# Kernel optimization log

Hardware: AMD Instinct MI355X
Metric: run time of the kernel (lower is better)

Reference implementation:

```python
import jax, jax.numpy as jnp
import numpy as np

V = 10000   # vocab size
H = 768     # HIDDEN_SIZE
B = 8       # batch
S = 512     # padded seq len
L = 8       # TRANSFORMER_LAYERS
EPS = 1e-5  # torch LayerNorm default eps


def setup_inputs() -> dict:
    key = jax.random.key(0)
    ks = jax.random.split(key, 16)
    init = lambda k, shape: jax.random.normal(k, shape, jnp.float32) * 0.02
    x = jax.random.randint(ks[0], (B, S), 0, V)
    # full-length sequences: avoids NaN from the original's softmax(dim=1) over
    # fully -inf padded columns (same behavior as torch for this input)
    lengths = jnp.full((B,), S, dtype=jnp.int32)
    return {
        'x': x,
        'lengths': lengths,
        'emb_w': init(ks[1], (V, H)),
        'Wq': init(ks[2], (L, H, H)), 'bq': jnp.zeros((L, H), jnp.float32),
        'Wk': init(ks[3], (L, H, H)), 'bk': jnp.zeros((L, H), jnp.float32),
        'Wv': init(ks[4], (L, H, H)), 'bv': jnp.zeros((L, H), jnp.float32),
        'W1': init(ks[5], (L, H, H)), 'b1': jnp.zeros((L, H), jnp.float32),
        'W2': init(ks[6], (L, H, H)), 'b2': jnp.zeros((L, H), jnp.float32),
        'g1': jnp.ones((L, H), jnp.float32), 'be1': jnp.zeros((L, H), jnp.float32),
        'g2': jnp.ones((L, H), jnp.float32), 'be2': jnp.zeros((L, H), jnp.float32),
        'fc_w': init(ks[7], (H, H)), 'fc_b': jnp.zeros((H,), jnp.float32),
    }


def _layernorm(x, g, b):
    m = jnp.mean(x, axis=-1, keepdims=True)
    v = jnp.mean(jnp.square(x - m), axis=-1, keepdims=True)
    return (x - m) * jax.lax.rsqrt(v + EPS) * g + b


def _pos_encoding(seq, dim):
    pos = jnp.arange(seq, dtype=jnp.float32)[:, None]
    div = jnp.exp(jnp.arange(0, dim, 2, dtype=jnp.float32) * (-np.log(10000.0) / dim))
    ang = pos * div[None, :]                                  # [S, H/2]
    return jnp.stack([jnp.sin(ang), jnp.cos(ang)], axis=-1).reshape(seq, dim)


def reference(x, lengths, emb_w, Wq, bq, Wk, bk, Wv, bv, W1, b1, W2, b2,
              g1, be1, g2, be2, fc_w, fc_b):
    z = emb_w[x] + _pos_encoding(S, H)[None]                  # [B,S,H]
    causal = jnp.tril(jnp.ones((S, S), bool))                 # [S,S]
    valid = jnp.arange(S)[None, :] < lengths[:, None]         # [B,S]
    mask = causal[None] & valid[:, None, :] & valid[:, :, None]  # [B,S,S]
    scale = 1.0 / jnp.sqrt(jnp.float32(H))
    for i in range(L):
        q = z @ Wq[i] + bq[i]
        k = z @ Wk[i] + bk[i]
        v = z @ Wv[i] + bv[i]
        scores = jnp.einsum('bqh,bkh->bqk', q, k) * scale
        scores = jnp.where(mask, scores, -jnp.inf)
        # NOTE: original code applies softmax over dim=1 (query axis) — faithful
        atten = jax.nn.softmax(scores, axis=1)
        out = jnp.einsum('bqk,bkh->bqh', atten, v)
        o1 = _layernorm(z + out, g1[i], be1[i])               # eval: dropout=identity
        mid = jax.nn.relu(o1 @ W1[i] + b1[i]) @ W2[i] + b2[i]
        z = _layernorm(mid + o1, g2[i], be2[i])
    zf = z @ fc_w + fc_b                                      # [B,S,H]
    logits = jnp.einsum('bsh,vh->bsv', zf, emb_w)             # [B,S,V]
    return jax.nn.softmax(logits, axis=-1)
```

## Files before the change

### kernel.cpp

```cpp
#include <hip/hip_runtime.h>
#include <math.h>

typedef unsigned int   u32;
typedef unsigned short u16;
typedef __attribute__((ext_vector_type(8))) short bf16x8;
typedef __attribute__((ext_vector_type(4))) float f32x4;
typedef __attribute__((ext_vector_type(4))) unsigned short u16x4;
typedef __attribute__((ext_vector_type(8))) unsigned short u16x8;

#define HID   768
#define SEQ   512
#define BATCH 8
#define LAYERS 8
#define VOC   10000
#define NROWS (BATCH*SEQ)
#define NH    ((long long)NROWS*HID)
#define SS8   ((long long)BATCH*SEQ*SEQ)
#define EPSLN 1e-5f
#define WSZ   ((long long)HID*HID)

__device__ __forceinline__ u16 f2bf(float f) {
    u32 u = __builtin_bit_cast(u32, f);
    return (u16)((u + 0x7fffu + ((u >> 16) & 1u)) >> 16);
}
__device__ __forceinline__ float bf2f(u16 h) {
    return __builtin_bit_cast(float, (u32)h << 16);
}

__device__ __forceinline__ void async16(u16* lds, const u16* g) {
    __builtin_amdgcn_global_load_lds(
        (const __attribute__((address_space(1))) u32*)g,
        (__attribute__((address_space(3))) u32*)lds, 16, 0, 0);
}

__global__ __launch_bounds__(256) void embed_kernel(
    const int* __restrict__ x, const float* __restrict__ emb,
    float* __restrict__ Z, u16* __restrict__ Zh)
{
    const int row = blockIdx.x;
    const int s   = row & (SEQ - 1);
    const int tok = x[row];
    const long long base  = (long long)row * HID;
    const long long ebase = (long long)tok * HID;
    const float coef = -0.0239852613853544f;
    #pragma unroll
    for (int j = 0; j < 3; ++j) {
        const int h = threadIdx.x + 256 * j;
        const int i = h >> 1;
        const float ang = (float)s * expf((float)i * coef);
        const float pe  = (h & 1) ? cosf(ang) : sinf(ang);
        const float v = emb[ebase + h] + pe;
        Z[base + h]  = v;
        Zh[base + h] = f2bf(v);
    }
}

__global__ __launch_bounds__(256) void convert_emb(
    const float* __restrict__ e, u16* __restrict__ eh)
{
    const long long i = ((long long)blockIdx.x * 256 + threadIdx.x) * 4;
    const float4 v = *(const float4*)&e[i];
    u16x4 p;
    p[0] = f2bf(v.x); p[1] = f2bf(v.y); p[2] = f2bf(v.z); p[3] = f2bf(v.w);
    *(u16x4*)&eh[i] = p;
}

__global__ __launch_bounds__(256) void transp_all(
    const float* __restrict__ Wq, const float* __restrict__ Wk,
    const float* __restrict__ Wv, const float* __restrict__ W1,
    const float* __restrict__ W2, const float* __restrict__ fcw,
    u16* __restrict__ WT)
{
    __shared__ u16 tile[32][34];
    const int z = blockIdx.z;
    const float* src;
    long long doff;
    if (z < 40) {
        const int lyr = z / 5, idx = z % 5;
        const float* bases[5] = {Wq, Wk, Wv, W1, W2};
        src  = bases[idx] + (long long)lyr * WSZ;
        doff = ((long long)lyr * 5 + idx) * WSZ;
    } else {
        src = fcw; doff = 40LL * WSZ;
    }
    u16* D = WT + doff;
    const int n0 = blockIdx.x * 32, k0 = blockIdx.y * 32;
    const int c = threadIdx.x & 31, r0 = threadIdx.x >> 5;
    #pragma unroll
    for (int p = 0; p < 4; ++p)
        tile[r0 + 8*p][c] = f2bf(src[(long long)(k0 + r0 + 8*p) * HID + n0 + c]);
    __syncthreads();
    #pragma unroll
    for (int p = 0; p < 4; ++p)
        D[(long long)(n0 + r0 + 8*p) * HID + k0 + c] = tile[c][r0 + 8*p];
}

__global__ void pack_bias_all(const float* __restrict__ bq,
                              const float* __restrict__ bk,
                              const float* __restrict__ bv,
                              float* __restrict__ dst)
{
    const int part = blockIdx.x, l = blockIdx.y, h = threadIdx.x;
    const float* src = part == 0 ? bq : (part == 1 ? bk : bv);
    dst[((long long)l*3 + part) * HID + h] = src[(long long)l*HID + h];
}

template<bool VSPLIT>
__global__ __launch_bounds__(512) void gemm_8ph(
    const u16* __restrict__ A, const u16* __restrict__ B,
    u16* __restrict__ Cp, int ldc, int N, int K,
    const float* __restrict__ bias, u16* __restrict__ vt)
{
    __shared__ u16 Ab[2][2][8192];
    __shared__ u16 Bb[2][2][8192];
    const int m0 = blockIdx.x * 256;
    const int n0 = blockIdx.y * 256;
    const int t = threadIdx.x, w = t >> 6, l = t & 63;
    const int fr = l & 15, jl = l >> 4;
    const int wm = (w >> 2) * 128, wn = (w & 3) * 64;

    f32x4 acc[8][4];
    #pragma unroll
    for (int mf = 0; mf < 8; ++mf)
        #pragma unroll
        for (int nf = 0; nf < 4; ++nf) acc[mf][nf] = (f32x4){0.f,0.f,0.f,0.f};

    auto stageA = [&](int d, int h, int kt) {
        #pragma unroll
        for (int r = 0; r < 2; ++r) {
            const int f16 = r * 512 + t;
            const int row = f16 >> 2, j = f16 & 3;
            const int kofs = kt + h * 32 + ((j ^ ((row >> 1) & 3)) << 3);
            async16(&Ab[d][h][f16 * 8], A + (long long)(m0 + row) * K + kofs);
        }
    };
    auto stageB = [&](int d, int h, int kt) {
        #pragma unroll
        for (int r = 0; r < 2; ++r) {
            const int f16 = r * 512 + t;
            const int row = f16 >> 2, j = f16 & 3;
            int gr = n0 + row; gr = gr < N ? gr : N - 1;
            const int kofs = kt + h * 32 + ((j ^ ((row >> 1) & 3)) << 3);
            async16(&Bb[d][h][f16 * 8], B + (long long)gr * K + kofs);
        }
    };

    stageA(0, 0, 0); stageB(0, 0, 0); stageA(0, 1, 0); stageB(0, 1, 0);

    const int NT = K >> 6;
    for (int tt = 0; tt < NT; ++tt) {
        const int d = tt & 1, kt1 = (tt + 1) << 6;
        const bool more = (tt + 1) < NT;
        #pragma unroll
        for (int h = 0; h < 2; ++h) {
            if (h == 0 || more) asm volatile("s_waitcnt vmcnt(4)" ::: "memory");
            else                asm volatile("s_waitcnt vmcnt(0)" ::: "memory");
            __builtin_amdgcn_s_barrier();
            asm volatile("" ::: "memory");
            if (more) stageA(d ^ 1, h, kt1);
            bf16x8 bfr[4], af[4];
            #pragma unroll
            for (int nf = 0; nf < 4; ++nf) {
                const int row = wn + nf * 16 + fr;
                bfr[nf] = *(const bf16x8*)
                    &Bb[d][h][row * 32 + ((jl ^ ((row >> 1) & 3)) << 3)];
            }
            #pragma unroll
            for (int mi = 0; mi < 4; ++mi) {
                const int row = wm + mi * 16 + fr;
                af[mi] = *(const bf16x8*)
                    &Ab[d][h][row * 32 + ((jl ^ ((row >> 1) & 3)) << 3)];
            }
            __builtin_amdgcn_s_setprio(1);
            #pragma unroll
            for (int mi = 0; mi < 4; ++mi)
                #pragma unroll
                for (int nf = 0; nf < 4; ++nf)
                    acc[mi][nf] = __builtin_amdgcn_mfma_f32_16x16x32_bf16(
                        af[mi], bfr[nf], acc[mi][nf], 0, 0, 0);
            __builtin_amdgcn_s_setprio(0);
            if (more) stageB(d ^ 1, h, kt1);
            #pragma unroll
            for (int mi = 0; mi < 4; ++mi) {
                const int row = wm + (mi + 4) * 16 + fr;
                af[mi] = *(const bf16x8*)
                    &Ab[d][h][row * 32 + ((jl ^ ((row >> 1) & 3)) << 3)];
            }
            __builtin_amdgcn_s_setprio(1);
            #pragma unroll
            for (int mi = 0; mi < 4; ++mi)
                #pragma unroll
                for (int nf = 0; nf < 4; ++nf)
                    acc[mi + 4][nf] = __builtin_amdgcn_mfma_f32_16x16x32_bf16(
                        af[mi], bfr[nf], acc[mi + 4][nf], 0, 0, 0);
            __builtin_amdgcn_s_setprio(0);
        }
    }

    #pragma unroll
    for (int nf = 0; nf < 4; ++nf) {
        const int col = n0 + wn + nf * 16 + fr;
        if (col >= N) continue;
        const float bv = bias ? bias[col] : 0.f;
        #pragma unroll
        for (int mf = 0; mf < 8; ++mf) {
            const int row0 = m0 + wm + mf * 16 + jl * 4;
            if constexpr (VSPLIT) {
                if (col < 1536) {
                    #pragma unroll
                    for (int v = 0; v < 4; ++v)
                        Cp[(long long)(row0 + v) * ldc + col] =
                            f2bf(acc[mf][nf][v] + bv);
                } else {
                    const int b9 = row0 >> 9, s9 = row0 & 511;
                    u16x4 pk;
                    #pragma unroll
                    for (int v = 0; v < 4; ++v)
                        pk[v] = f2bf(acc[mf][nf][v] + bv);
                    *(u16x4*)&vt[((long long)b9 * HID + (col - 1536)) * SEQ + s9] = pk;
                }
            } else {
                #pragma unroll
                for (int v = 0; v < 4; ++v)
                    Cp[(long long)(row0 + v) * ldc + col] =
                        f2bf(acc[mf][nf][v] + bv);
            }
        }
    }
}

template<bool RELU, bool OUT_BF16>
__global__ __launch_bounds__(128) void gemm_small(
    const u16* __restrict__ A, int lda, long long sA,
    const u16* __restrict__ B, int ldb, long long sB,
    void* __restrict__ Cp, int ldc, long long sC,
    int N, int K, const float* __restrict__ bias, float alpha)
{
    __shared__ u16 As[2][64 * 64];
    __shared__ u16 Bs[2][64 * 64];
    const int bz = blockIdx.z;
    const int n0 = blockIdx.x * 64;
    const int m0 = blockIdx.y * 64;
    const int t = threadIdx.x, w = t >> 6, l = t & 63;
    const int srow = l >> 3;
    const int skof = ((l & 7) ^ srow) * 8;
    const int wm = w * 32;
    A += sA * bz; B += sB * bz;

    f32x4 acc[2][4];
    #pragma unroll
    for (int mi = 0; mi < 2; ++mi)
        #pragma unroll
        for (int ni = 0; ni < 4; ++ni) acc[mi][ni] = (f32x4){0.f,0.f,0.f,0.f};

    auto stage = [&](int buf, int k0) {
        #pragma unroll
        for (int r = 0; r < 4; ++r) {
            const int seg = w * 4 + r;
            const int row = seg * 8 + srow;
            async16(&As[buf][seg * 512],
                    A + (long long)(m0 + row) * lda + (k0 + skof));
        }
        #pragma unroll
        for (int r = 0; r < 4; ++r) {
            const int seg = w * 4 + r;
            const int row = seg * 8 + srow;
            async16(&Bs[buf][seg * 512],
                    B + (long long)(n0 + row) * ldb + (k0 + skof));
        }
    };
    const int fr = l & 15, fkb = l >> 4;
    auto compute = [&](int cur) {
        #pragma unroll
        for (int ks = 0; ks < 2; ++ks) {
            const int ps = ((ks * 4 + fkb) ^ (fr & 7)) * 8;
            bf16x8 af[2], bfv[4];
            #pragma unroll
            for (int mi = 0; mi < 2; ++mi)
                af[mi] = *(const bf16x8*)&As[cur][(wm + mi*16 + fr) * 64 + ps];
            #pragma unroll
            for (int ni = 0; ni < 4; ++ni)
                bfv[ni] = *(const bf16x8*)&Bs[cur][(ni*16 + fr) * 64 + ps];
            #pragma unroll
            for (int mi = 0; mi < 2; ++mi)
                #pragma unroll
                for (int ni = 0; ni < 4; ++ni)
                    acc[mi][ni] = __builtin_amdgcn_mfma_f32_16x16x32_bf16(
                        af[mi], bfv[ni], acc[mi][ni], 0, 0, 0);
        }
    };

    const int NS = K >> 6;
    stage(0, 0);
    for (int tt = 0; tt < NS; ++tt) {
        if (tt + 1 < NS) {
            stage((tt + 1) & 1, (tt + 1) << 6);
            asm volatile("s_waitcnt vmcnt(8)\n\ts_barrier" ::: "memory");
        } else {
            asm volatile("s_waitcnt vmcnt(0)\n\ts_barrier" ::: "memory");
        }
        compute(tt & 1);
        asm volatile("s_barrier" ::: "memory");
    }

    float* Cf = (float*)Cp + sC * bz;
    u16*   Ch = (u16*)Cp + sC * bz;
    const int fq = l >> 4;
    #pragma unroll
    for (int ni = 0; ni < 4; ++ni) {
        const int col = n0 + ni*16 + fr;
        const float bv = bias ? bias[col] : 0.f;
        #pragma unroll
        for (int mi = 0; mi < 2; ++mi) {
            const int row0 = m0 + wm + mi*16 + fq*4;
            #pragma unroll
            for (int v = 0; v < 4; ++v) {
                float val = alpha * acc[mi][ni][v] + bv;
                if (RELU) val = fmaxf(val, 0.f);
                if (OUT_BF16) Ch[(long long)(row0 + v) * ldc + col] = f2bf(val);
                else          Cf[(long long)(row0 + v) * ldc + col] = val;
            }
        }
    }
}

__global__ __launch_bounds__(256) void gemm_conv(
    const u16* __restrict__ A, const float* __restrict__ Bf,
    u16* __restrict__ C)
{
    __shared__ u16 As[128 * 32];
    __shared__ u16 Bs[128 * 32];
    const int m0 = blockIdx.x * 128;
    const int n0 = blockIdx.y * 128;
    const int t = threadIdx.x, w = t >> 6, l = t & 63;
    const int lrow = l >> 2, lk8 = (l & 3) * 8;
    const int wm = (w >> 1) * 64, wn = (w & 1) * 64;
    f32x4 acc[4][4];
    #pragma unroll
    for (int mi = 0; mi < 4; ++mi)
        #pragma unroll
        for (int ni = 0; ni < 4; ++ni) acc[mi][ni] = (f32x4){0.f,0.f,0.f,0.f};

    for (int k0 = 0; k0 < HID; k0 += 32) {
        #pragma unroll
        for (int r = 0; r < 2; ++r) {
            const int seg = w * 2 + r;
            async16(&As[seg * 512],
                    A + (long long)(m0 + seg*16 + lrow) * HID + (k0 + lk8));
        }
        #pragma unroll
        for (int r = 0; r < 2; ++r) {
            const int flat = r * 2048 + t * 8;
            int row = n0 + (flat >> 5);
            row = row < VOC ? row : VOC - 1;
            const float* g = Bf + (long long)row * HID + (k0 + (flat & 31));
            const float4 v0 = *(const float4*)g;
            const float4 v1 = *(const float4*)(g + 4);
            bf16x8 hv;
            hv[0]=(short)f2bf(v0.x); hv[1]=(short)f2bf(v0.y);
            hv[2]=(short)f2bf(v0.z); hv[3]=(short)f2bf(v0.w);
            hv[4]=(short)f2bf(v1.x); hv[5]=(short)f2bf(v1.y);
            hv[6]=(short)f2bf(v1.z); hv[7]=(short)f2bf(v1.w);
            *(bf16x8*)&Bs[flat] = hv;
        }
        __syncthreads();
        const int fr = l & 15, fk = (l >> 4) * 8;
        bf16x8 af[4], bfr[4];
        #pragma unroll
        for (int mi = 0; mi < 4; ++mi)
            af[mi] = *(const bf16x8*)&As[(wm + mi*16 + fr) * 32 + fk];
        #pragma unroll
        for (int ni = 0; ni < 4; ++ni)
            bfr[ni] = *(const bf16x8*)&Bs[(wn + ni*16 + fr) * 32 + fk];
        #pragma unroll
        for (int mi = 0; mi < 4; ++mi)
            #pragma unroll
            for (int ni = 0; ni < 4; ++ni)
                acc[mi][ni] = __builtin_amdgcn_mfma_f32_16x16x32_bf16(
                    af[mi], bfr[ni], acc[mi][ni], 0, 0, 0);
        __syncthreads();
    }
    const int fr = l & 15, fq = l >> 4;
    #pragma unroll
    for (int ni = 0; ni < 4; ++ni) {
        const int col = n0 + wn + ni*16 + fr;
        if (col >= VOC) continue;
        #pragma unroll
        for (int mi = 0; mi < 4; ++mi) {
            const int row0 = m0 + wm + mi*16 + fq*4;
            #pragma unroll
            for (int v = 0; v < 4; ++v)
                C[(long long)(row0 + v) * (2*VOC) + col] = f2bf(acc[mi][ni][v]);
        }
    }
}

__global__ __launch_bounds__(256) void softmax_q_kernel(
    const float* __restrict__ sc, u16* __restrict__ att,
    const int* __restrict__ lengths)
{
    const int b  = blockIdx.x;
    const int k0 = blockIdx.y * 16;
    const int tx = threadIdx.x & 15;
    const int ty = threadIdx.x >> 4;
    const int c  = k0 + tx;
    const int len = lengths[b];
    const float* base  = sc  + (long long)b * SEQ * SEQ;
    u16*         obase = att + (long long)b * SEQ * SEQ;
    const bool cvalid = (c < len);

    float vals[32];
    float m = -3.0e38f, ssum = 0.f;
    #pragma unroll
    for (int i = 0; i < 32; ++i) {
        const int q = ty + 16 * i;
        float xv = -3.0e38f;
        if (cvalid && c <= q && q < len)
            xv = base[(long long)q * SEQ + c];
        vals[i] = xv;
        if (xv > m) { ssum = ssum * __expf(m - xv) + 1.f; m = xv; }
        else if (xv > -3.0e38f) { ssum += __expf(xv - m); }
    }
    __shared__ float ms[16][17], ss[16][17];
    ms[ty][tx] = m; ss[ty][tx] = ssum;
    __syncthreads();
    if (ty == 0) {
        float M = ms[0][tx];
        #pragma unroll
        for (int r = 1; r < 16; ++r) M = fmaxf(M, ms[r][tx]);
        float Sx = 0.f;
        #pragma unroll
        for (int r = 0; r < 16; ++r) Sx += ss[r][tx] * __expf(ms[r][tx] - M);
        ms[0][tx] = M; ss[0][tx] = Sx;
    }
    __syncthreads();
    const float M   = ms[0][tx];
    const float den = ss[0][tx];
    const float inv = (den > 0.f) ? 1.f / den : 0.f;
    #pragma unroll
    for (int i = 0; i < 32; ++i) {
        const int q = ty + 16 * i;
        obase[(long long)q * SEQ + c] = f2bf(__expf(vals[i] - M) * inv);
    }
}

__global__ __launch_bounds__(256) void ln_add_kernel(
    const float* __restrict__ Xa, const float* __restrict__ Xb,
    float* __restrict__ O, u16* __restrict__ Oh,
    const float* __restrict__ g, const float* __restrict__ be)
{
    const int row = blockIdx.x * 4 + (threadIdx.x >> 6);
    const int l = threadIdx.x & 63;
    const long long base = (long long)row * HID;
    float x[12];
    #pragma unroll
    for (int c = 0; c < 3; ++c) {
        const int off = c * 256 + l * 4;
        const float4 a = *(const float4*)&Xa[base + off];
        const float4 b = *(const float4*)&Xb[base + off];
        x[c*4+0] = a.x + b.x; x[c*4+1] = a.y + b.y;
        x[c*4+2] = a.z + b.z; x[c*4+3] = a.w + b.w;
    }
    float s = 0.f;
    #pragma unroll
    for (int i = 0; i < 12; ++i) s += x[i];
    #pragma unroll
    for (int o = 32; o; o >>= 1) s += __shfl_xor(s, o, 64);
    const float mean = s * (1.f / HID);
    float v = 0.f;
    #pragma unroll
    for (int i = 0; i < 12; ++i) { const float d = x[i] - mean; v += d * d; }
    #pragma unroll
    for (int o = 32; o; o >>= 1) v += __shfl_xor(v, o, 64);
    const float rs = rsqrtf(v * (1.f / HID) + EPSLN);
    #pragma unroll
    for (int c = 0; c < 3; ++c) {
        const int off = c * 256 + l * 4;
        const float4 gg = *(const float4*)&g[off];
        const float4 bb = *(const float4*)&be[off];
        float4 y;
        y.x = (x[c*4+0] - mean) * rs * gg.x + bb.x;
        y.y = (x[c*4+1] - mean) * rs * gg.y + bb.y;
        y.z = (x[c*4+2] - mean) * rs * gg.z + bb.z;
        y.w = (x[c*4+3] - mean) * rs * gg.w + bb.w;
        *(float4*)&O[base + off] = y;
        u16x4 p;
        p[0] = f2bf(y.x); p[1] = f2bf(y.y); p[2] = f2bf(y.z); p[3] = f2bf(y.w);
        *(u16x4*)&Oh[base + off] = p;
    }
}

__global__ __launch_bounds__(256) void softmax_v_kernel(float* __restrict__ out)
{
    __shared__ float row[VOC];
    __shared__ float rm[4], rs_[4];
    const long long obase = (long long)blockIdx.x * VOC;
    const u16* lg = (const u16*)out + 2 * obase + VOC;
    const int t = threadIdx.x;
    float m = -3.0e38f, s = 0.f;
    for (int i = t * 8; i < VOC; i += 2048) {
        const u16x8 h8 = *(const u16x8*)&lg[i];
        #pragma unroll
        for (int j = 0; j < 8; ++j) {
            const float xv = bf2f(h8[j]);
            row[i + j] = xv;
            const float d = xv - m;
            if (d > 0.f) { s = s * __expf(-d) + 1.f; m = xv; }
            else         { s += __expf(d); }
        }
    }
    #pragma unroll
    for (int o = 32; o; o >>= 1) {
        const float om = __shfl_down(m, o, 64), os = __shfl_down(s, o, 64);
        const float M = fmaxf(m, om);
        s = s * __expf(m - M) + os * __expf(om - M);
        m = M;
    }
    if ((t & 63) == 0) { rm[t >> 6] = m; rs_[t >> 6] = s; }
    __syncthreads();
    const float M = fmaxf(fmaxf(rm[0], rm[1]), fmaxf(rm[2], rm[3]));
    const float S = rs_[0]*__expf(rm[0]-M) + rs_[1]*__expf(rm[1]-M)
                  + rs_[2]*__expf(rm[2]-M) + rs_[3]*__expf(rm[3]-M);
    const float inv = 1.f / S;
    for (int i = t * 4; i < VOC; i += 1024) {
        float4 v = *(const float4*)&row[i];
        v.x = __expf(v.x - M) * inv;
        v.y = __expf(v.y - M) * inv;
        v.z = __expf(v.z - M) * inv;
        v.w = __expf(v.w - M) * inv;
        *(float4*)&out[obase + i] = v;
    }
}

extern "C" void kernel_launch(void* const* d_in, const int* in_sizes, int n_in,
                              void* d_out, int out_size, void* d_ws, size_t ws_size,
                              hipStream_t stream)
{
    const int*   x    = (const int*)  d_in[0];
    const int*   lens = (const int*)  d_in[1];
    const float* emb  = (const float*)d_in[2];
    const float* Wq   = (const float*)d_in[3];
    const float* bq   = (const float*)d_in[4];
    const float* Wk   = (const float*)d_in[5];
    const float* bk   = (const float*)d_in[6];
    const float* Wv   = (const float*)d_in[7];
    const float* bv   = (const float*)d_in[8];
    const float* W1   = (const float*)d_in[9];
    const float* b1   = (const float*)d_in[10];
    const float* W2   = (const float*)d_in[11];
    const float* b2   = (const float*)d_in[12];
    const float* g1   = (const float*)d_in[13];
    const float* be1  = (const float*)d_in[14];
    const float* g2   = (const float*)d_in[15];
    const float* be2  = (const float*)d_in[16];
    const float* fcw  = (const float*)d_in[17];
    const float* fcb  = (const float*)d_in[18];

    float* out = (float*)d_out;
    float* Zb     = out;
    float* O1f    = Zb + NH;
    float* M2f    = O1f + NH;
    float* SCORES = M2f + NH;
    float* BQKV   = SCORES + SS8;
    u16* ub   = (u16*)(BQKV + (long long)LAYERS * 2304);
    u16* Zbh  = ub;  ub += NH;
    u16* QKVh = ub;  ub += (long long)NROWS * 1536;
    u16* ATTB = ub;  ub += SS8;
    u16* Vt   = ub;  ub += NH;
    u16* O1h  = ub;  ub += NH;
    u16* M1h  = ub;  ub += NH;
    u16* WT   = ub;  ub += 41LL * WSZ;

    u16* ZFh = (u16*)d_ws;
    u16* EH  = ZFh + NH;
    const bool ehpath = ws_size >= (size_t)((NH + (long long)VOC * HID) * 2);
    u16* LOGH = (u16*)out + VOC;

    const float scale = 1.0f / sqrtf((float)HID);
    const dim3 blk(256), blk128(128), blk512(512);

    embed_kernel<<<NROWS, blk, 0, stream>>>(x, emb, Zb, Zbh);
    transp_all<<<dim3(24, 24, 41), blk, 0, stream>>>(Wq, Wk, Wv, W1, W2, fcw, WT);
    pack_bias_all<<<dim3(3, LAYERS), dim3(768), 0, stream>>>(bq, bk, bv, BQKV);
    if (ehpath) convert_emb<<<7500, blk, 0, stream>>>(emb, EH);

    for (int l = 0; l < LAYERS; ++l) {
        const u16* wl = WT + (long long)l * 5 * WSZ;

        gemm_8ph<true><<<dim3(16, 9), blk512, 0, stream>>>(
            Zbh, wl, QKVh, 1536, 2304, HID,
            BQKV + (long long)l * 2304, Vt);

        gemm_small<false, false><<<dim3(8, 8, BATCH), blk128, 0, stream>>>(
            QKVh, 1536, (long long)SEQ * 1536,
            QKVh + 768, 1536, (long long)SEQ * 1536,
            SCORES, SEQ, (long long)SEQ * SEQ,
            512, HID, nullptr, scale);

        softmax_q_kernel<<<dim3(BATCH, SEQ/16), blk, 0, stream>>>(SCORES, ATTB, lens);

        gemm_small<false, false><<<dim3(12, 8, BATCH), blk128, 0, stream>>>(
            ATTB, SEQ, (long long)SEQ * SEQ,
            Vt, SEQ, (long long)HID * SEQ,
            O1f, HID, (long long)SEQ * HID,
            768, SEQ, nullptr, 1.0f);

        ln_add_kernel<<<NROWS/4, blk, 0, stream>>>(Zb, O1f, O1f, O1h,
                                                   g1 + l*HID, be1 + l*HID);
        gemm_small<true, true><<<dim3(12, 64), blk128, 0, stream>>>(
            O1h, HID, 0, wl + 3*WSZ, HID, 0, M1h, HID, 0,
            768, HID, b1 + l*HID, 1.0f);
        gemm_small<false, false><<<dim3(12, 64), blk128, 0, stream>>>(
            M1h, HID, 0, wl + 4*WSZ, HID, 0, M2f, HID, 0,
            768, HID, b2 + l*HID, 1.0f);
        ln_add_kernel<<<NROWS/4, blk, 0, stream>>>(M2f, O1f, Zb, Zbh,
                                                   g2 + l*HID, be2 + l*HID);
    }

    gemm_small<false, true><<<dim3(12, 64), blk128, 0, stream>>>(
        Zbh, HID, 0, WT + 40LL*WSZ, HID, 0, ZFh, HID, 0,
        768, HID, fcb, 1.0f);

    if (ehpath) {
        gemm_8ph<false><<<dim3(16, 40), blk512, 0, stream>>>(
            ZFh, EH, LOGH, 2*VOC, VOC, HID, nullptr, nullptr);
    } else {
        gemm_conv<<<dim3(32, 79), blk, 0, stream>>>(ZFh, emb, LOGH);
    }

    softmax_v_kernel<<<NROWS, blk, 0, stream>>>(out);
}
```

Baseline: 1.143 ms.

## Replace 256x256 8-phase GEMM with 128x128 double-buffered GEMM and grid ordering

Replaces the 512-thread 256x256-tile GEMM used for the QKV projection and the vocab logits with a 256-thread 128x128-tile kernel. It stages full 64-wide K slices with an XOR swizzle and a simple double-buffered loop. A template flag picks whether blockIdx.x walks M or N to change tile rasterisation per call site. The smaller tiles give many more blocks (576 for QKV versus 144) for better CU occupancy, at the cost of lower data reuse per block and less finely interleaved prefetch.

After: 1.126 ms. About the same (-1.5%).

```diff
diff --git a/kernel.cpp b/kernel.cpp
--- a/kernel.cpp
+++ b/kernel.cpp
@@ -105,125 +105,111 @@
     dst[((long long)l*3 + part) * HID + h] = src[(long long)l*HID + h];
 }
 
-template<bool VSPLIT>
-__global__ __launch_bounds__(512) void gemm_8ph(
+template<bool XISM, bool VSPLIT>
+__global__ __launch_bounds__(256) void gemm_big(
     const u16* __restrict__ A, const u16* __restrict__ B,
     u16* __restrict__ Cp, int ldc, int N, int K,
     const float* __restrict__ bias, u16* __restrict__ vt)
 {
-    __shared__ u16 Ab[2][2][8192];
-    __shared__ u16 Bb[2][2][8192];
-    const int m0 = blockIdx.x * 256;
-    const int n0 = blockIdx.y * 256;
+    __shared__ u16 As[2][128 * 64];
+    __shared__ u16 Bs[2][128 * 64];
+    const int m0 = (XISM ? blockIdx.x : blockIdx.y) * 128;
+    const int n0 = (XISM ? blockIdx.y : blockIdx.x) * 128;
     const int t = threadIdx.x, w = t >> 6, l = t & 63;
-    const int fr = l & 15, jl = l >> 4;
-    const int wm = (w >> 2) * 128, wn = (w & 3) * 64;
-
-    f32x4 acc[8][4];
-    #pragma unroll
-    for (int mf = 0; mf < 8; ++mf)
-        #pragma unroll
-        for (int nf = 0; nf < 4; ++nf) acc[mf][nf] = (f32x4){0.f,0.f,0.f,0.f};
-
-    auto stageA = [&](int d, int h, int kt) {
-        #pragma unroll
-        for (int r = 0; r < 2; ++r) {
-            const int f16 = r * 512 + t;
-            const int row = f16 >> 2, j = f16 & 3;
-            const int kofs = kt + h * 32 + ((j ^ ((row >> 1) & 3)) << 3);
-            async16(&Ab[d][h][f16 * 8], A + (long long)(m0 + row) * K + kofs);
+    const int wm = (w >> 1) * 64, wn = (w & 1) * 64;
+
+    f32x4 acc[4][4];
+    #pragma unroll
+    for (int mi = 0; mi < 4; ++mi)
+        #pragma unroll
+        for (int ni = 0; ni < 4; ++ni) acc[mi][ni] = (f32x4){0.f,0.f,0.f,0.f};
+
+    auto stage = [&](int buf, int kt) {
+        #pragma unroll
+        for (int r = 0; r < 4; ++r) {
+            const int f = r * 256 + t;
+            const int row = f >> 3, j = f & 7;
+            async16(&As[buf][f * 8],
+                    A + (long long)(m0 + row) * K + kt + ((j ^ (row & 7)) << 3));
+        }
+        #pragma unroll
+        for (int r = 0; r < 4; ++r) {
+            const int f = r * 256 + t;
+            const int row = f >> 3, j = f & 7;
+            int gr = n0 + row; gr = gr < N ? gr : N - 1;
+            async16(&Bs[buf][f * 8],
+                    B + (long long)gr * K + kt + ((j ^ (row & 7)) << 3));
         }
     };
-    auto stageB = [&](int d, int h, int kt) {
-        #pragma unroll
-        for (int r = 0; r < 2; ++r) {
-            const int f16 = r * 512 + t;
-            const int row = f16 >> 2, j = f16 & 3;
-            int gr = n0 + row; gr = gr < N ? gr : N - 1;
-            const int kofs = kt + h * 32 + ((j ^ ((row >> 1) & 3)) << 3);
-            async16(&Bb[d][h][f16 * 8], B + (long long)gr * K + kofs);
-        }
-    };
-
-    stageA(0, 0, 0); stageB(0, 0, 0); stageA(0, 1, 0); stageB(0, 1, 0);
-
-    const int NT = K >> 6;
-    for (int tt = 0; tt < NT; ++tt) {
-        const int d = tt & 1, kt1 = (tt + 1) << 6;
-        const bool more = (tt + 1) < NT;
-        #pragma unroll
-        for (int h = 0; h < 2; ++h) {
-            if (h == 0 || more) asm volatile("s_waitcnt vmcnt(4)" ::: "memory");
-            else                asm volatile("s_waitcnt vmcnt(0)" ::: "memory");
-            __builtin_amdgcn_s_barrier();
-            asm volatile("" ::: "memory");
-            if (more) stageA(d ^ 1, h, kt1);
-            bf16x8 bfr[4], af[4];
-            #pragma unroll
-            for (int nf = 0; nf < 4; ++nf) {
-                const int row = wn + nf * 16 + fr;
-                bfr[nf] = *(const bf16x8*)
-                    &Bb[d][h][row * 32 + ((jl ^ ((row >> 1) & 3)) << 3)];
+    const int fr = l & 15, fk = l >> 4;
+    auto compute = [&](int cur) {
+        #pragma unroll
+        for (int ks = 0; ks < 2; ++ks) {
+            bf16x8 af[4], bfr[4];
+            #pragma unroll
+            for (int mi = 0; mi < 4; ++mi) {
+                const int row = wm + mi*16 + fr;
+                af[mi] = *(const bf16x8*)
+                    &As[cur][row * 64 + (((ks*4 + fk) ^ (row & 7)) << 3)];
             }
             #pragma unroll
-            for (int mi = 0; mi < 4; ++mi) {
-                const int row = wm + mi * 16 + fr;
-                af[mi] = *(const bf16x8*)
-                    &Ab[d][h][row * 32 + ((jl ^ ((row >> 1) & 3)) << 3)];
+            for (int ni = 0; ni < 4; ++ni) {
+                const int row = wn + ni*16 + fr;
+                bfr[ni] = *(const bf16x8*)
+                    &Bs[cur][row * 64 + (((ks*4 + fk) ^ (row & 7)) << 3)];
             }
             __builtin_amdgcn_s_setprio(1);
             #pragma unroll
             for (int mi = 0; mi < 4; ++mi)
                 #pragma unroll
-                for (int nf = 0; nf < 4; ++nf)
-                    acc[mi][nf] = __builtin_amdgcn_mfma_f32_16x16x32_bf16(
-                        af[mi], bfr[nf], acc[mi][nf], 0, 0, 0);
+                for (int ni = 0; ni < 4; ++ni)
+                    acc[mi][ni] = __builtin_amdgcn_mfma_f32_16x16x32_bf16(
+                        af[mi], bfr[ni], acc[mi][ni], 0, 0, 0);
             __builtin_amdgcn_s_setprio(0);
-            if (more) stageB(d ^ 1, h, kt1);
-            #pragma unroll
-            for (int mi = 0; mi < 4; ++mi) {
-                const int row = wm + (mi + 4) * 16 + fr;
-                af[mi] = *(const bf16x8*)
-                    &Ab[d][h][row * 32 + ((jl ^ ((row >> 1) & 3)) << 3)];
-            }
-            __builtin_amdgcn_s_setprio(1);
-            #pragma unroll
-            for (int mi = 0; mi < 4; ++mi)
-                #pragma unroll
-                for (int nf = 0; nf < 4; ++nf)
-                    acc[mi + 4][nf] = __builtin_amdgcn_mfma_f32_16x16x32_bf16(
-                        af[mi], bfr[nf], acc[mi + 4][nf], 0, 0, 0);
-            __builtin_amdgcn_s_setprio(0);
-        }
-    }
-
-    #pragma unroll
-    for (int nf = 0; nf < 4; ++nf) {
-        const int col = n0 + wn + nf * 16 + fr;
+        }
+    };
+
+    const int NS = K >> 6;
+    stage(0, 0);
+    for (int tt = 0; tt < NS; ++tt) {
+        if (tt + 1 < NS) {
+            stage((tt + 1) & 1, (tt + 1) << 6);
+            asm volatile("s_waitcnt vmcnt(8)\n\ts_barrier" ::: "memory");
+        } else {
+            asm volatile("s_waitcnt vmcnt(0)\n\ts_barrier" ::: "memory");
+        }
+        compute(tt & 1);
+        asm volatile("s_barrier" ::: "memory");
+    }
+
+    const int fq = l >> 4;
+    #pragma unroll
+    for (int ni = 0; ni < 4; ++ni) {
+        const int col = n0 + wn + ni*16 + fr;
         if (col >= N) continue;
         const float bv = bias ? bias[col] : 0.f;
         #pragma unroll
-        for (int mf = 0; mf < 8; ++mf) {
-            const int row0 = m0 + wm + mf * 16 + jl * 4;
+        for (int mi = 0; mi < 4; ++mi) {
+            const int row0 = m0 + wm + mi*16 + fq*4;
             if constexpr (VSPLIT) {
                 if (col < 1536) {
                     #pragma unroll
                     for (int v = 0; v < 4; ++v)
                         Cp[(long long)(row0 + v) * ldc + col] =
-                            f2bf(acc[mf][nf][v] + bv);
+                            f2bf(acc[mi][ni][v] + bv);
                 } else {
                     const int b9 = row0 >> 9, s9 = row0 & 511;
                     u16x4 pk;
                     #pragma unroll
                     for (int v = 0; v < 4; ++v)
-                        pk[v] = f2bf(acc[mf][nf][v] + bv);
+                        pk[v] = f2bf(acc[mi][ni][v] + bv);
                     *(u16x4*)&vt[((long long)b9 * HID + (col - 1536)) * SEQ + s9] = pk;
                 }
             } else {
                 #pragma unroll
                 for (int v = 0; v < 4; ++v)
                     Cp[(long long)(row0 + v) * ldc + col] =
-                        f2bf(acc[mf][nf][v] + bv);
+                        f2bf(acc[mi][ni][v] + bv);
             }
         }
     }
@@ -577,7 +563,7 @@
     u16* LOGH = (u16*)out + VOC;
 
     const float scale = 1.0f / sqrtf((float)HID);
-    const dim3 blk(256), blk128(128), blk512(512);
+    const dim3 blk(256), blk128(128);
 
     embed_kernel<<<NROWS, blk, 0, stream>>>(x, emb, Zb, Zbh);
     transp_all<<<dim3(24, 24, 41), blk, 0, stream>>>(Wq, Wk, Wv, W1, W2, fcw, WT);
@@ -587,7 +573,7 @@
     for (int l = 0; l < LAYERS; ++l) {
         const u16* wl = WT + (long long)l * 5 * WSZ;
 
-        gemm_8ph<true><<<dim3(16, 9), blk512, 0, stream>>>(
+        gemm_big<false, true><<<dim3(18, 32), blk, 0, stream>>>(
             Zbh, wl, QKVh, 1536, 2304, HID,
             BQKV + (long long)l * 2304, Vt);
 
@@ -622,7 +608,7 @@
         768, HID, fcb, 1.0f);
 
     if (ehpath) {
-        gemm_8ph<false><<<dim3(16, 40), blk512, 0, stream>>>(
+        gemm_big<true, false><<<dim3(32, 79), blk, 0, stream>>>(
             ZFh, EH, LOGH, 2*VOC, VOC, HID, nullptr, nullptr);
     } else {
         gemm_conv<<<dim3(32, 79), blk, 0, stream>>>(ZFh, emb, LOGH);
```

## Template GEMM tile height and deepen async pipeline to three stages ahead

Applied to the files above, without the earlier changes.

The 8-phase GEMM now takes the M tile size as a template parameter, so the QKV projection can use 128-row tiles and launch twice as many blocks (32x9). The main loop is restructured into per-32-K phases with prefetch issued three phases ahead and vmcnt-based waits, replacing the earlier two-half double-buffer schedule. This aims to fill more CUs for the small QKV GEMM and hide more global load latency. The cost is more barriers per K step and a simpler MFMA/load interleave within each phase, which may lose some of the previous overlap.

After: 1.250 ms. +9.4%, slower.

```diff
diff --git a/kernel.cpp b/kernel.cpp
--- a/kernel.cpp
+++ b/kernel.cpp
@@ -105,96 +105,84 @@
     dst[((long long)l*3 + part) * HID + h] = src[(long long)l*HID + h];
 }
 
-template<bool VSPLIT>
+template<int BM, bool VSPLIT>
 __global__ __launch_bounds__(512) void gemm_8ph(
     const u16* __restrict__ A, const u16* __restrict__ B,
     u16* __restrict__ Cp, int ldc, int N, int K,
     const float* __restrict__ bias, u16* __restrict__ vt)
 {
-    __shared__ u16 Ab[2][2][8192];
-    __shared__ u16 Bb[2][2][8192];
-    const int m0 = blockIdx.x * 256;
+    constexpr int MF = BM / 128;
+    constexpr int MI = BM / 32;
+    __shared__ u16 Ab[2][2][BM * 32];
+    __shared__ u16 Bb[2][2][256 * 32];
+    const int m0 = blockIdx.x * BM;
     const int n0 = blockIdx.y * 256;
     const int t = threadIdx.x, w = t >> 6, l = t & 63;
     const int fr = l & 15, jl = l >> 4;
-    const int wm = (w >> 2) * 128, wn = (w & 3) * 64;
-
-    f32x4 acc[8][4];
-    #pragma unroll
-    for (int mf = 0; mf < 8; ++mf)
+    const int wm = (w >> 2) * (BM / 2), wn = (w & 3) * 64;
+
+    f32x4 acc[MI][4];
+    #pragma unroll
+    for (int mf = 0; mf < MI; ++mf)
         #pragma unroll
         for (int nf = 0; nf < 4; ++nf) acc[mf][nf] = (f32x4){0.f,0.f,0.f,0.f};
 
-    auto stageA = [&](int d, int h, int kt) {
+    auto stageA = [&](int g) {
+        const int d = (g >> 1) & 1, h = g & 1, kt = (g >> 1) << 6;
+        #pragma unroll
+        for (int r = 0; r < MF; ++r) {
+            const int c = r * 512 + t;
+            const int row = c >> 2, j = c & 3;
+            const int kof = kt + h * 32 + ((j ^ ((row >> 1) & 3)) << 3);
+            async16(&Ab[d][h][c * 8], A + (long long)(m0 + row) * K + kof);
+        }
+    };
+    auto stageB = [&](int g) {
+        const int d = (g >> 1) & 1, h = g & 1, kt = (g >> 1) << 6;
         #pragma unroll
         for (int r = 0; r < 2; ++r) {
-            const int f16 = r * 512 + t;
-            const int row = f16 >> 2, j = f16 & 3;
-            const int kofs = kt + h * 32 + ((j ^ ((row >> 1) & 3)) << 3);
-            async16(&Ab[d][h][f16 * 8], A + (long long)(m0 + row) * K + kofs);
+            const int c = r * 512 + t;
+            const int row = c >> 2, j = c & 3;
+            int gr = n0 + row; gr = gr < N ? gr : N - 1;
+            const int kof = kt + h * 32 + ((j ^ ((row >> 1) & 3)) << 3);
+            async16(&Bb[d][h][c * 8], B + (long long)gr * K + kof);
         }
     };
-    auto stageB = [&](int d, int h, int kt) {
-        #pragma unroll
-        for (int r = 0; r < 2; ++r) {
-            const int f16 = r * 512 + t;
-            const int row = f16 >> 2, j = f16 & 3;
-            int gr = n0 + row; gr = gr < N ? gr : N - 1;
-            const int kofs = kt + h * 32 + ((j ^ ((row >> 1) & 3)) << 3);
-            async16(&Bb[d][h][f16 * 8], B + (long long)gr * K + kofs);
-        }
-    };
-
-    stageA(0, 0, 0); stageB(0, 0, 0); stageA(0, 1, 0); stageB(0, 1, 0);
-
-    const int NT = K >> 6;
-    for (int tt = 0; tt < NT; ++tt) {
-        const int d = tt & 1, kt1 = (tt + 1) << 6;
-        const bool more = (tt + 1) < NT;
-        #pragma unroll
-        for (int h = 0; h < 2; ++h) {
-            if (h == 0 || more) asm volatile("s_waitcnt vmcnt(4)" ::: "memory");
-            else                asm volatile("s_waitcnt vmcnt(0)" ::: "memory");
-            __builtin_amdgcn_s_barrier();
-            asm volatile("" ::: "memory");
-            if (more) stageA(d ^ 1, h, kt1);
-            bf16x8 bfr[4], af[4];
+
+    const int P = K >> 5;
+    stageA(0); stageB(0); stageA(1); stageB(1); stageA(2); stageB(2);
+    for (int ph = 0; ph < P; ++ph) {
+        const int rem = P - 1 - ph;
+        if (rem >= 2)
+            asm volatile("s_waitcnt vmcnt(%0)" :: "i"(2 * (MF + 2)) : "memory");
+        else if (rem == 1)
+            asm volatile("s_waitcnt vmcnt(%0)" :: "i"(MF + 2) : "memory");
+        else
+            asm volatile("s_waitcnt vmcnt(0)" ::: "memory");
+        __builtin_amdgcn_s_barrier();
+        if (ph + 3 < P) { stageA(ph + 3); stageB(ph + 3); }
+        const int d = (ph >> 1) & 1, h = ph & 1;
+        bf16x8 bfr[4], af[MI];
+        #pragma unroll
+        for (int nf = 0; nf < 4; ++nf) {
+            const int row = wn + nf * 16 + fr;
+            bfr[nf] = *(const bf16x8*)
+                &Bb[d][h][row * 32 + ((jl ^ ((row >> 1) & 3)) << 3)];
+        }
+        #pragma unroll
+        for (int mf = 0; mf < MI; ++mf) {
+            const int row = wm + mf * 16 + fr;
+            af[mf] = *(const bf16x8*)
+                &Ab[d][h][row * 32 + ((jl ^ ((row >> 1) & 3)) << 3)];
+        }
+        __builtin_amdgcn_s_setprio(1);
+        #pragma unroll
+        for (int mf = 0; mf < MI; ++mf)
             #pragma unroll
-            for (int nf = 0; nf < 4; ++nf) {
-                const int row = wn + nf * 16 + fr;
-                bfr[nf] = *(const bf16x8*)
-                    &Bb[d][h][row * 32 + ((jl ^ ((row >> 1) & 3)) << 3)];
-            }
-            #pragma unroll
-            for (int mi = 0; mi < 4; ++mi) {
-                const int row = wm + mi * 16 + fr;
-                af[mi] = *(const bf16x8*)
-                    &Ab[d][h][row * 32 + ((jl ^ ((row >> 1) & 3)) << 3)];
-            }
-            __builtin_amdgcn_s_setprio(1);
-            #pragma unroll
-            for (int mi = 0; mi < 4; ++mi)
-                #pragma unroll
-                for (int nf = 0; nf < 4; ++nf)
-                    acc[mi][nf] = __builtin_amdgcn_mfma_f32_16x16x32_bf16(
-                        af[mi], bfr[nf], acc[mi][nf], 0, 0, 0);
-            __builtin_amdgcn_s_setprio(0);
-            if (more) stageB(d ^ 1, h, kt1);
-            #pragma unroll
-            for (int mi = 0; mi < 4; ++mi) {
-                const int row = wm + (mi + 4) * 16 + fr;
-                af[mi] = *(const bf16x8*)
-                    &Ab[d][h][row * 32 + ((jl ^ ((row >> 1) & 3)) << 3)];
-            }
-            __builtin_amdgcn_s_setprio(1);
-            #pragma unroll
-            for (int mi = 0; mi < 4; ++mi)
-                #pragma unroll
-                for (int nf = 0; nf < 4; ++nf)
-                    acc[mi + 4][nf] = __builtin_amdgcn_mfma_f32_16x16x32_bf16(
-                        af[mi], bfr[nf], acc[mi + 4][nf], 0, 0, 0);
-            __builtin_amdgcn_s_setprio(0);
-        }
+            for (int nf = 0; nf < 4; ++nf)
+                acc[mf][nf] = __builtin_amdgcn_mfma_f32_16x16x32_bf16(
+                    af[mf], bfr[nf], acc[mf][nf], 0, 0, 0);
+        __builtin_amdgcn_s_setprio(0);
     }
 
     #pragma unroll
@@ -203,7 +191,7 @@
         if (col >= N) continue;
         const float bv = bias ? bias[col] : 0.f;
         #pragma unroll
-        for (int mf = 0; mf < 8; ++mf) {
+        for (int mf = 0; mf < MI; ++mf) {
             const int row0 = m0 + wm + mf * 16 + jl * 4;
             if constexpr (VSPLIT) {
                 if (col < 1536) {
@@ -587,7 +575,7 @@
     for (int l = 0; l < LAYERS; ++l) {
         const u16* wl = WT + (long long)l * 5 * WSZ;
 
-        gemm_8ph<true><<<dim3(16, 9), blk512, 0, stream>>>(
+        gemm_8ph<128, true><<<dim3(32, 9), blk512, 0, stream>>>(
             Zbh, wl, QKVh, 1536, 2304, HID,
             BQKV + (long long)l * 2304, Vt);
 
@@ -622,7 +610,7 @@
         768, HID, fcb, 1.0f);
 
     if (ehpath) {
-        gemm_8ph<false><<<dim3(16, 40), blk512, 0, stream>>>(
+        gemm_8ph<256, false><<<dim3(16, 40), blk512, 0, stream>>>(
             ZFh, EH, LOGH, 2*VOC, VOC, HID, nullptr, nullptr);
     } else {
         gemm_conv<<<dim3(32, 79), blk, 0, stream>>>(ZFh, emb, LOGH);
```
